# Kernel optimization log

Hardware: AMD Instinct MI355X
Metric: run time of the kernel (lower is better)

Reference implementation:

```python
import jax, jax.numpy as jnp
import numpy as np

EPS = 1e-12  # matches torch F.normalize eps


def _l2_normalize(x, axis):
    n = jnp.sqrt(jnp.sum(x * x, axis=axis, keepdims=True))
    return x / jnp.maximum(n, EPS)


def setup_inputs() -> dict:
    key = jax.random.key(0)
    k1, k2 = jax.random.split(key)
    phi = jax.random.normal(k1, (64, 512), dtype=jnp.float32)          # (m, H)
    psi = jax.random.normal(k2, (64, 1024, 512), dtype=jnp.float32)    # (m, n, W)
    return {"phi": phi, "psi": psi}


def reference(phi, psi):
    phi = phi.astype(jnp.float32)
    psi = psi.astype(jnp.float32)
    m, H = phi.shape
    m2, n, W = psi.shape
    phi = _l2_normalize(phi, axis=1)   # rows of phi
    psi = _l2_normalize(psi, axis=2)   # each measurement vector

    g_phi_sq = jnp.square(phi @ phi.T)  # (m, m)

    # b[i, j] = sum_{u,v} (psi[i,u] . psi[j,v])^2 = ||psi_i psi_j^T||_F^2
    #         = <psi_i^T psi_i, psi_j^T psi_j>_F  (exact identity, avoids (m,m,n,n))
    S = jnp.einsum('inw,inv->iwv', psi, psi)   # (m, W, W) per-block Gram
    b = jnp.einsum('iwv,jwv->ij', S, S)        # (m, m)

    loss = jnp.sum(g_phi_sq * b) - jnp.float32(m * n)
    return loss
```

## Files before the change

### kernel.cpp

```cpp
#include <hip/hip_runtime.h>
#include <hip/hip_bf16.h>

typedef unsigned short u16;
typedef unsigned int u32;
typedef __attribute__((ext_vector_type(8))) short short8x;
typedef __attribute__((ext_vector_type(4))) float f32x4;

__device__ __forceinline__ u16 bf16u(float x) {
    __hip_bfloat16 h = __float2bfloat16(x);
    return *reinterpret_cast<u16*>(&h);
}

__device__ __forceinline__ void gload_lds16(const void* g, void* l) {
    __builtin_amdgcn_global_load_lds(
        (const __attribute__((address_space(1))) u32*)g,
        (__attribute__((address_space(3))) u32*)l, 16, 0, 0);
}

#define M_  64
#define N_  1024
#define W_  512
#define SP_ROW 163840

__global__ __launch_bounds__(256) void psinorm_t(const float* __restrict__ psi,
                                                 u16* __restrict__ psiT) {
    const int i  = blockIdx.y;
    const int nb = blockIdx.x;
    const int t  = threadIdx.x;
    const float* base = psi + ((size_t)i * N_ + (size_t)nb * 64) * W_;

    __shared__ u32 tile[64][257];

    const int sub = t & 15;

#pragma unroll
    for (int pp = 0; pp < 4; ++pp) {
        const int r = pp * 16 + (t >> 4);
        const float4* rb = (const float4*)(base + (size_t)r * W_) + sub;
        float4 v[8];
        float s = 0.f;
#pragma unroll
        for (int k = 0; k < 8; ++k) {
            v[k] = rb[k * 16];
            s += v[k].x * v[k].x + v[k].y * v[k].y + v[k].z * v[k].z + v[k].w * v[k].w;
        }
#pragma unroll
        for (int o = 1; o < 16; o <<= 1) s += __shfl_xor(s, o);
        const float inv = 1.0f / fmaxf(sqrtf(s), 1e-12f);
#pragma unroll
        for (int k = 0; k < 8; ++k) {
            u32 p0 = (u32)bf16u(v[k].x * inv) | ((u32)bf16u(v[k].y * inv) << 16);
            u32 p1 = (u32)bf16u(v[k].z * inv) | ((u32)bf16u(v[k].w * inv) << 16);
            const int wh = sub * 2 + k * 32;
            tile[r][wh]     = p0;
            tile[r][wh + 1] = p1;
        }
    }
    __syncthreads();

    {
        const u16* t16 = (const u16*)&tile[0][0];
        const int lane = t & 63, wv = t >> 6;
        const int q  = lane & 31;
        const int l5 = lane >> 5;
        u32* out32 = (u32*)psiT + (size_t)i * (W_ * N_ / 2) + nb * 32;
#pragma unroll 4
        for (int it = 0; it < 64; ++it) {
            const int w = it * 8 + wv * 2 + l5;
            u32 lo = (u32)t16[(2 * q)     * 514 + w];
            u32 hi = (u32)t16[(2 * q + 1) * 514 + w];
            out32[(size_t)w * 512 + q] = lo | (hi << 16);
        }
    }
}

__global__ __launch_bounds__(256) void syrk_bf16(const u16* __restrict__ psiT,
                                                 u16* __restrict__ Sp) {
    const int L = blockIdx.x;
    const int q = L >> 3;
    const int i  = (L & 7) * 8 + q / 10;
    const int bt = q % 10;
    int tr, tc;
    if      (bt < 4) { tr = 0; tc = bt;     }
    else if (bt < 7) { tr = 1; tc = bt - 3; }
    else if (bt < 9) { tr = 2; tc = bt - 5; }
    else             { tr = 3; tc = 3;      }
    const int t = threadIdx.x;

    const u16* Abase = psiT + (size_t)i * W_ * N_ + (size_t)tr * 128 * N_;
    const u16* Bbase = psiT + (size_t)i * W_ * N_ + (size_t)tc * 128 * N_;

    __shared__ alignas(16) u16 ldsA[2][128][64];
    __shared__ alignas(16) u16 ldsB[2][128][64];

    const int lane = t & 63, wv = t >> 6;
    const int wr = wv >> 1, wc = wv & 1;
    const int lrow = lane & 15, lk8 = lane >> 4;

    auto STAGE = [&](int buf, int kt) {
        const int k0 = kt * 64;
#pragma unroll
        for (int r = 0; r < 4; ++r) {
            int c = r * 256 + t;
            int row = c >> 3, cch = c & 7;
            int scch = cch ^ (row & 7);
            gload_lds16(Abase + (size_t)row * N_ + k0 + scch * 8, &ldsA[buf][row][cch * 8]);
            gload_lds16(Bbase + (size_t)row * N_ + k0 + scch * 8, &ldsB[buf][row][cch * 8]);
        }
    };

    f32x4 acc[4][4];
#pragma unroll
    for (int a = 0; a < 4; ++a)
#pragma unroll
        for (int b = 0; b < 4; ++b) acc[a][b] = (f32x4){0.f, 0.f, 0.f, 0.f};

    STAGE(0, 0);
    asm volatile("s_waitcnt vmcnt(0)" ::: "memory");
    __builtin_amdgcn_s_barrier();

    int cur = 0;
    for (int kt = 0; kt < 16; ++kt) {
        if (kt < 15) STAGE(cur ^ 1, kt + 1);
#pragma unroll
        for (int ks = 0; ks < 2; ++ks) {
            short8x af[4], bf[4];
#pragma unroll
            for (int mf = 0; mf < 4; ++mf) {
                int row = wr * 64 + mf * 16 + lrow;
                int ch = (ks * 4 + lk8) ^ (row & 7);
                af[mf] = *(const short8x*)&ldsA[cur][row][ch * 8];
            }
#pragma unroll
            for (int nf = 0; nf < 4; ++nf) {
                int row = wc * 64 + nf * 16 + lrow;
                int ch = (ks * 4 + lk8) ^ (row & 7);
                bf[nf] = *(const short8x*)&ldsB[cur][row][ch * 8];
            }
#pragma unroll
            for (int mf = 0; mf < 4; ++mf)
#pragma unroll
                for (int nf = 0; nf < 4; ++nf)
                    acc[mf][nf] = __builtin_amdgcn_mfma_f32_16x16x32_bf16(
                        af[mf], bf[nf], acc[mf][nf], 0, 0, 0);
        }
        asm volatile("s_waitcnt vmcnt(0)" ::: "memory");
        __builtin_amdgcn_sched_barrier(0);
        __builtin_amdgcn_s_barrier();
        cur ^= 1;
    }

    const float sc = (tr == tc) ? 1.0f : 1.41421356237f;
    size_t Sbase = (size_t)i * SP_ROW + (size_t)bt * 16384;
#pragma unroll
    for (int mf = 0; mf < 4; ++mf)
#pragma unroll
        for (int nf = 0; nf < 4; ++nf)
#pragma unroll
            for (int reg = 0; reg < 4; ++reg) {
                int wl = wr * 64 + mf * 16 + lk8 * 4 + reg;
                int vl = wc * 64 + nf * 16 + lrow;
                Sp[Sbase + (size_t)wl * 128 + vl] = bf16u(acc[mf][nf][reg] * sc);
            }
}

__global__ __launch_bounds__(256) void bgemm(const u16* __restrict__ Sp,
                                             float* __restrict__ bp) {
    const int t = threadIdx.x;
    const int lane = t & 63, wv = t >> 6;
    const int wr = wv >> 1, wc = wv & 1;
    const int lrow = lane & 15, lk8 = lane >> 4;
    const size_t kc0 = (size_t)blockIdx.x * 256;

    f32x4 acc[2][2];
#pragma unroll
    for (int a = 0; a < 2; ++a)
#pragma unroll
        for (int b = 0; b < 2; ++b) acc[a][b] = (f32x4){0.f, 0.f, 0.f, 0.f};

#pragma unroll
    for (int ks = 0; ks < 8; ++ks) {
        short8x af[2], bf[2];
#pragma unroll
        for (int mf = 0; mf < 2; ++mf) {
            int row = wr * 32 + mf * 16 + lrow;
            af[mf] = *(const short8x*)(Sp + (size_t)row * SP_ROW + kc0 + (ks * 4 + lk8) * 8);
        }
#pragma unroll
        for (int nf = 0; nf < 2; ++nf) {
            int row = wc * 32 + nf * 16 + lrow;
            bf[nf] = *(const short8x*)(Sp + (size_t)row * SP_ROW + kc0 + (ks * 4 + lk8) * 8);
        }
#pragma unroll
        for (int mf = 0; mf < 2; ++mf)
#pragma unroll
            for (int nf = 0; nf < 2; ++nf)
                acc[mf][nf] = __builtin_amdgcn_mfma_f32_16x16x32_bf16(
                    af[mf], bf[nf], acc[mf][nf], 0, 0, 0);
    }

    float* out = bp + (size_t)blockIdx.x * 4096;
#pragma unroll
    for (int mf = 0; mf < 2; ++mf)
#pragma unroll
        for (int nf = 0; nf < 2; ++nf)
#pragma unroll
            for (int reg = 0; reg < 4; ++reg) {
                int ir = wr * 32 + mf * 16 + lk8 * 4 + reg;
                int jc = wc * 32 + nf * 16 + lrow;
                out[ir * 64 + jc] = acc[mf][nf][reg];
            }
}

__global__ __launch_bounds__(256) void bfinal(const float* __restrict__ bp,
                                              const float* __restrict__ phi,
                                              float* __restrict__ parts) {
    const int i = blockIdx.x, t = threadIdx.x;
    const int lane = t & 63, wv = t >> 6;

    __shared__ float red[256];
    __shared__ float brow[64];
    __shared__ float pi[512];
    __shared__ float dj[64], nsq[64];

    {
        float s = 0.f;
        for (int p = wv; p < 640; p += 4) s += bp[(size_t)p * 4096 + i * 64 + lane];
        red[t] = s;
    }
    pi[t] = phi[i * 512 + t];
    pi[t + 256] = phi[i * 512 + 256 + t];
    __syncthreads();
    if (t < 64) brow[t] = red[t] + red[64 + t] + red[128 + t] + red[192 + t];

    for (int jj = 0; jj < 16; ++jj) {
        int j = wv + jj * 4;
        const float* pj = phi + j * 512;
        float d = 0.f, nn = 0.f;
#pragma unroll
        for (int e = 0; e < 8; ++e) {
            float x = pj[lane + e * 64];
            d += pi[lane + e * 64] * x;
            nn += x * x;
        }
#pragma unroll
        for (int o = 32; o; o >>= 1) {
            d += __shfl_xor(d, o);
            nn += __shfl_xor(nn, o);
        }
        if (lane == 0) { dj[j] = d; nsq[j] = nn; }
    }
    __syncthreads();
    if (t < 64) {
        float ni = fmaxf(sqrtf(nsq[i]), 1e-12f);
        float nj = fmaxf(sqrtf(nsq[t]), 1e-12f);
        float g = dj[t] / (ni * nj);
        float val = g * g * brow[t];
#pragma unroll
        for (int o = 32; o; o >>= 1) val += __shfl_down(val, o);
        if (t == 0) parts[i] = val;
    }
}

__global__ void fsum(const float* __restrict__ parts, float* __restrict__ out) {
    const int t = threadIdx.x;
    float s = parts[t];
#pragma unroll
    for (int o = 32; o; o >>= 1) s += __shfl_down(s, o);
    if (t == 0) out[0] = s - 65536.0f;
}

__global__ void wsfail(float* __restrict__ out) {
    if (threadIdx.x == 0) out[0] = 1.0e30f;
}

extern "C" void kernel_launch(void* const* d_in, const int* in_sizes, int n_in,
                              void* d_out, int out_size, void* d_ws, size_t ws_size,
                              hipStream_t stream) {
    const float* phi = (const float*)d_in[0];
    const float* psi = (const float*)d_in[1];
    float* out = (float*)d_out;
    char* ws = (char*)d_ws;

    const size_t NEEDED = 67108864ull + 20971520ull + 256ull;
    if (ws_size < NEEDED) {
        wsfail<<<1, 64, 0, stream>>>(out);
        return;
    }
    u16*   psiT  = (u16*)(ws);
    float* bp    = (float*)(ws);
    u16*   Sp    = (u16*)(ws + 67108864);
    float* parts = (float*)(ws + 88080384);

    psinorm_t<<<dim3(16, 64), 256, 0, stream>>>(psi, psiT);
    syrk_bf16<<<640,          256, 0, stream>>>(psiT, Sp);
    bgemm    <<<640,          256, 0, stream>>>(Sp, bp);
    bfinal   <<<64,           256, 0, stream>>>(bp, phi, parts);
    fsum     <<<1,            64,  0, stream>>>(parts, out);
}
```

Measured before the change: 311.5 us.

## Fuse phi Gram into normalize kernel and weighted reduction into bgemm

Moves the phi Gram computation into 16 extra blocks of the psi normalize/transpose kernel, which write squared normalized Gram values to a small buffer and initialise the output. The bgemm kernel now weights its partial b tile by that buffer and atomically adds a scalar to the output. This drops the 10 MB partial-b write and read, plus the bfinal and fsum launches. In exchange the final sum uses 640 float atomics, so its order is no longer deterministic.

```diff
diff --git a/kernel.cpp b/kernel.cpp
--- a/kernel.cpp
+++ b/kernel.cpp
@@ -23,42 +23,45 @@
 #define SP_ROW 163840
 
 __global__ __launch_bounds__(256) void psinorm_t(const float* __restrict__ psi,
-                                                 u16* __restrict__ psiT) {
-    const int i  = blockIdx.y;
-    const int nb = blockIdx.x;
-    const int t  = threadIdx.x;
-    const float* base = psi + ((size_t)i * N_ + (size_t)nb * 64) * W_;
-
+                                                 const float* __restrict__ phi,
+                                                 u16* __restrict__ psiT,
+                                                 float* __restrict__ g2,
+                                                 float* __restrict__ out) {
+    const int t = threadIdx.x;
     __shared__ u32 tile[64][257];
-
-    const int sub = t & 15;
-
-#pragma unroll
-    for (int pp = 0; pp < 4; ++pp) {
-        const int r = pp * 16 + (t >> 4);
-        const float4* rb = (const float4*)(base + (size_t)r * W_) + sub;
-        float4 v[8];
-        float s = 0.f;
-#pragma unroll
-        for (int k = 0; k < 8; ++k) {
-            v[k] = rb[k * 16];
-            s += v[k].x * v[k].x + v[k].y * v[k].y + v[k].z * v[k].z + v[k].w * v[k].w;
-        }
-#pragma unroll
-        for (int o = 1; o < 16; o <<= 1) s += __shfl_xor(s, o);
-        const float inv = 1.0f / fmaxf(sqrtf(s), 1e-12f);
-#pragma unroll
-        for (int k = 0; k < 8; ++k) {
-            u32 p0 = (u32)bf16u(v[k].x * inv) | ((u32)bf16u(v[k].y * inv) << 16);
-            u32 p1 = (u32)bf16u(v[k].z * inv) | ((u32)bf16u(v[k].w * inv) << 16);
-            const int wh = sub * 2 + k * 32;
-            tile[r][wh]     = p0;
-            tile[r][wh + 1] = p1;
-        }
-    }
-    __syncthreads();
-
-    {
+    __shared__ float djs[4][64], nsqs[64];
+
+    if (blockIdx.x < 1024) {
+        const int i  = blockIdx.x >> 4;
+        const int nb = blockIdx.x & 15;
+        const float* base = psi + ((size_t)i * N_ + (size_t)nb * 64) * W_;
+        const int sub = t & 15;
+
+#pragma unroll
+        for (int pp = 0; pp < 4; ++pp) {
+            const int r = pp * 16 + (t >> 4);
+            const float4* rb = (const float4*)(base + (size_t)r * W_) + sub;
+            float4 v[8];
+            float s = 0.f;
+#pragma unroll
+            for (int k = 0; k < 8; ++k) {
+                v[k] = rb[k * 16];
+                s += v[k].x * v[k].x + v[k].y * v[k].y + v[k].z * v[k].z + v[k].w * v[k].w;
+            }
+#pragma unroll
+            for (int o = 1; o < 16; o <<= 1) s += __shfl_xor(s, o);
+            const float inv = 1.0f / fmaxf(sqrtf(s), 1e-12f);
+#pragma unroll
+            for (int k = 0; k < 8; ++k) {
+                u32 p0 = (u32)bf16u(v[k].x * inv) | ((u32)bf16u(v[k].y * inv) << 16);
+                u32 p1 = (u32)bf16u(v[k].z * inv) | ((u32)bf16u(v[k].w * inv) << 16);
+                const int wh = sub * 2 + k * 32;
+                tile[r][wh]     = p0;
+                tile[r][wh + 1] = p1;
+            }
+        }
+        __syncthreads();
+
         const u16* t16 = (const u16*)&tile[0][0];
         const int lane = t & 63, wv = t >> 6;
         const int q  = lane & 31;
@@ -71,6 +74,56 @@
             u32 hi = (u32)t16[(2 * q + 1) * 514 + w];
             out32[(size_t)w * 512 + q] = lo | (hi << 16);
         }
+    } else {
+        const int gb = blockIdx.x - 1024;
+        const int i0 = gb * 4;
+        const int lane = t & 63, wv = t >> 6;
+        float* pis = (float*)&tile[0][0];
+#pragma unroll
+        for (int r = 0; r < 4; ++r) {
+            pis[r * 512 + t]       = phi[(i0 + r) * 512 + t];
+            pis[r * 512 + 256 + t] = phi[(i0 + r) * 512 + 256 + t];
+        }
+        __syncthreads();
+
+        for (int jj = 0; jj < 16; ++jj) {
+            int j = wv + jj * 4;
+            const float* pj = phi + j * 512;
+            float nn = 0.f, d0 = 0.f, d1 = 0.f, d2 = 0.f, d3 = 0.f;
+#pragma unroll
+            for (int e = 0; e < 8; ++e) {
+                float x = pj[lane + e * 64];
+                nn += x * x;
+                d0 += pis[0 * 512 + lane + e * 64] * x;
+                d1 += pis[1 * 512 + lane + e * 64] * x;
+                d2 += pis[2 * 512 + lane + e * 64] * x;
+                d3 += pis[3 * 512 + lane + e * 64] * x;
+            }
+#pragma unroll
+            for (int o = 32; o; o >>= 1) {
+                nn += __shfl_xor(nn, o);
+                d0 += __shfl_xor(d0, o);
+                d1 += __shfl_xor(d1, o);
+                d2 += __shfl_xor(d2, o);
+                d3 += __shfl_xor(d3, o);
+            }
+            if (lane == 0) {
+                djs[0][j] = d0; djs[1][j] = d1; djs[2][j] = d2; djs[3][j] = d3;
+                nsqs[j] = nn;
+            }
+        }
+        __syncthreads();
+        if (t < 64) {
+            const int j = t;
+            const float invj = 1.0f / fmaxf(sqrtf(nsqs[j]), 1e-12f);
+#pragma unroll
+            for (int r = 0; r < 4; ++r) {
+                const float invi = 1.0f / fmaxf(sqrtf(nsqs[i0 + r]), 1e-12f);
+                const float g = djs[r][j] * invi * invj;
+                g2[(i0 + r) * 64 + j] = g * g;
+            }
+        }
+        if (gb == 0 && t == 0) out[0] = -65536.0f;
     }
 }
 
@@ -164,8 +217,9 @@
             }
 }
 
-__global__ __launch_bounds__(256) void bgemm(const u16* __restrict__ Sp,
-                                             float* __restrict__ bp) {
+__global__ __launch_bounds__(256) void bgemm_w(const u16* __restrict__ Sp,
+                                               const float* __restrict__ g2,
+                                               float* __restrict__ out) {
     const int t = threadIdx.x;
     const int lane = t & 63, wv = t >> 6;
     const int wr = wv >> 1, wc = wv & 1;
@@ -199,75 +253,24 @@
                     af[mf], bf[nf], acc[mf][nf], 0, 0, 0);
     }
 
-    float* out = bp + (size_t)blockIdx.x * 4096;
+    float wsum = 0.f;
 #pragma unroll
     for (int mf = 0; mf < 2; ++mf)
 #pragma unroll
-        for (int nf = 0; nf < 2; ++nf)
+        for (int nf = 0; nf < 2; ++nf) {
+            const int jc = wc * 32 + nf * 16 + lrow;
 #pragma unroll
             for (int reg = 0; reg < 4; ++reg) {
-                int ir = wr * 32 + mf * 16 + lk8 * 4 + reg;
-                int jc = wc * 32 + nf * 16 + lrow;
-                out[ir * 64 + jc] = acc[mf][nf][reg];
-            }
-}
-
-__global__ __launch_bounds__(256) void bfinal(const float* __restrict__ bp,
-                                              const float* __restrict__ phi,
-                                              float* __restrict__ parts) {
-    const int i = blockIdx.x, t = threadIdx.x;
-    const int lane = t & 63, wv = t >> 6;
-
-    __shared__ float red[256];
-    __shared__ float brow[64];
-    __shared__ float pi[512];
-    __shared__ float dj[64], nsq[64];
-
-    {
-        float s = 0.f;
-        for (int p = wv; p < 640; p += 4) s += bp[(size_t)p * 4096 + i * 64 + lane];
-        red[t] = s;
-    }
-    pi[t] = phi[i * 512 + t];
-    pi[t + 256] = phi[i * 512 + 256 + t];
+                const int ir = wr * 32 + mf * 16 + lk8 * 4 + reg;
+                wsum += acc[mf][nf][reg] * g2[ir * 64 + jc];
+            }
+        }
+#pragma unroll
+    for (int o = 32; o; o >>= 1) wsum += __shfl_down(wsum, o);
+    __shared__ float w4[4];
+    if (lane == 0) w4[wv] = wsum;
     __syncthreads();
-    if (t < 64) brow[t] = red[t] + red[64 + t] + red[128 + t] + red[192 + t];
-
-    for (int jj = 0; jj < 16; ++jj) {
-        int j = wv + jj * 4;
-        const float* pj = phi + j * 512;
-        float d = 0.f, nn = 0.f;
-#pragma unroll
-        for (int e = 0; e < 8; ++e) {
-            float x = pj[lane + e * 64];
-            d += pi[lane + e * 64] * x;
-            nn += x * x;
-        }
-#pragma unroll
-        for (int o = 32; o; o >>= 1) {
-            d += __shfl_xor(d, o);
-            nn += __shfl_xor(nn, o);
-        }
-        if (lane == 0) { dj[j] = d; nsq[j] = nn; }
-    }
-    __syncthreads();
-    if (t < 64) {
-        float ni = fmaxf(sqrtf(nsq[i]), 1e-12f);
-        float nj = fmaxf(sqrtf(nsq[t]), 1e-12f);
-        float g = dj[t] / (ni * nj);
-        float val = g * g * brow[t];
-#pragma unroll
-        for (int o = 32; o; o >>= 1) val += __shfl_down(val, o);
-        if (t == 0) parts[i] = val;
-    }
-}
-
-__global__ void fsum(const float* __restrict__ parts, float* __restrict__ out) {
-    const int t = threadIdx.x;
-    float s = parts[t];
-#pragma unroll
-    for (int o = 32; o; o >>= 1) s += __shfl_down(s, o);
-    if (t == 0) out[0] = s - 65536.0f;
+    if (t == 0) atomicAdd(out, w4[0] + w4[1] + w4[2] + w4[3]);
 }
 
 __global__ void wsfail(float* __restrict__ out) {
@@ -282,19 +285,16 @@
     float* out = (float*)d_out;
     char* ws = (char*)d_ws;
 
-    const size_t NEEDED = 67108864ull + 20971520ull + 256ull;
+    const size_t NEEDED = 67108864ull + 20971520ull + 16384ull;
     if (ws_size < NEEDED) {
         wsfail<<<1, 64, 0, stream>>>(out);
         return;
     }
-    u16*   psiT  = (u16*)(ws);
-    float* bp    = (float*)(ws);
-    u16*   Sp    = (u16*)(ws + 67108864);
-    float* parts = (float*)(ws + 88080384);
-
-    psinorm_t<<<dim3(16, 64), 256, 0, stream>>>(psi, psiT);
-    syrk_bf16<<<640,          256, 0, stream>>>(psiT, Sp);
-    bgemm    <<<640,          256, 0, stream>>>(Sp, bp);
-    bfinal   <<<64,           256, 0, stream>>>(bp, phi, parts);
-    fsum     <<<1,            64,  0, stream>>>(parts, out);
-}
+    u16*   psiT = (u16*)(ws);
+    u16*   Sp   = (u16*)(ws + 67108864);
+    float* g2   = (float*)(ws + 88080384);
+
+    psinorm_t<<<1040, 256, 0, stream>>>(psi, phi, psiT, g2, out);
+    syrk_bf16<<<640,  256, 0, stream>>>(psiT, Sp);
+    bgemm_w  <<<640,  256, 0, stream>>>(Sp, g2, out);
+}
```

Measured after the change: 268.8 us. 13.7% less time.
